# Optimization experiments

Measured on AMD Instinct MI355X. Metric: run time of the kernel, lower is better.

The kernel has to match this reference:

```python
import jax, jax.numpy as jnp
import numpy as np

NS, NM, NR, H = 5000, 100000, 2000, 128
E_SM, E_RM, E_SIM, L = 2_000_000, 1_000_000, 2_000_000, 500_000
NUM_LAYERS = 4  # flattened: layer-0 sage convs 0..3, layer-1 sage convs 0..3 -> stacked [2,4,...]


def _seg_sum(x, idx, n):
    return jax.ops.segment_sum(x, idx, num_segments=n)


def sage_conv(x_src, x_dst, Wl, bl, Wr, src, dst, n_dst):
    # PyG SAGEConv: mean-aggregate neighbor features, lin_l (with bias), + lin_r(root, no bias)
    agg = _seg_sum(x_src[src], dst, n_dst)                      # [n_dst, H]
    cnt = _seg_sum(jnp.ones_like(src, dtype=x_src.dtype), dst, n_dst)
    mean = agg / jnp.maximum(cnt, 1.0)[:, None]
    return mean @ Wl + bl + x_dst @ Wr


def gcn_conv(x, W, b, src, dst, n):
    # PyG GCNConv: add self loops, symmetric normalization deg^-1/2 (deg over dst incl. self loops)
    loop = jnp.arange(n, dtype=src.dtype)
    src2 = jnp.concatenate([src, loop])
    dst2 = jnp.concatenate([dst, loop])
    deg = _seg_sum(jnp.ones_like(dst2, dtype=x.dtype), dst2, n)
    dinv = jnp.where(deg > 0, jax.lax.rsqrt(deg), 0.0)
    norm = dinv[src2] * dinv[dst2]                               # [E+n]
    xw = x @ W                                                   # [n, H]
    out = _seg_sum(xw[src2] * norm[:, None], dst2, n)
    return out + b


def setup_inputs() -> dict:
    key = jax.random.key(0)
    ks = jax.random.split(key, 20)
    s = 0.05
    inp = {
        "emb_srna": jax.random.normal(ks[0], (NS, H), jnp.float32) * s,
        "emb_mrna": jax.random.normal(ks[1], (NM, H), jnp.float32) * s,
        "emb_rbp": jax.random.normal(ks[2], (NR, H), jnp.float32) * s,
        # stacked SAGE params: [layer=2, rel=4, ...]; rel order:
        # 0: srna->mrna, 1: mrna->srna (rev), 2: rbp->mrna, 3: mrna->rbp (rev)
        "sage_Wl": jax.random.normal(ks[3], (2, 4, H, H), jnp.float32) * s,
        "sage_bl": jnp.zeros((2, 4, H), jnp.float32),
        "sage_Wr": jax.random.normal(ks[4], (2, 4, H, H), jnp.float32) * s,
        # stacked GCN params: [layer=2, rel=2 (sim, rev_sim), ...]
        "gcn_W": jax.random.normal(ks[5], (2, 2, H, H), jnp.float32) * s,
        "gcn_b": jnp.zeros((2, 2, H), jnp.float32),
        "src_sm": jax.random.randint(ks[6], (E_SM,), 0, NS),
        "dst_sm": jax.random.randint(ks[7], (E_SM,), 0, NM),
        "src_rm": jax.random.randint(ks[8], (E_RM,), 0, NR),
        "dst_rm": jax.random.randint(ks[9], (E_RM,), 0, NM),
        "src_sim": jax.random.randint(ks[10], (E_SIM,), 0, NM),
        "dst_sim": jax.random.randint(ks[11], (E_SIM,), 0, NM),
        "lbl_srna": jax.random.randint(ks[12], (L,), 0, NS),
        "lbl_mrna": jax.random.randint(ks[13], (L,), 0, NM),
        "lbl_rbp": jax.random.randint(ks[14], (L,), 0, NR),
    }
    return inp


def reference(emb_srna, emb_mrna, emb_rbp, sage_Wl, sage_bl, sage_Wr, gcn_W, gcn_b,
              src_sm, dst_sm, src_rm, dst_rm, src_sim, dst_sim,
              lbl_srna, lbl_mrna, lbl_rbp):
    x_s, x_m, x_r = emb_srna, emb_mrna, emb_rbp
    for l in range(2):
        m_new = (
            sage_conv(x_s, x_m, sage_Wl[l, 0], sage_bl[l, 0], sage_Wr[l, 0], src_sm, dst_sm, NM)
            + sage_conv(x_r, x_m, sage_Wl[l, 2], sage_bl[l, 2], sage_Wr[l, 2], src_rm, dst_rm, NM)
            + gcn_conv(x_m, gcn_W[l, 0], gcn_b[l, 0], src_sim, dst_sim, NM)
            + gcn_conv(x_m, gcn_W[l, 1], gcn_b[l, 1], dst_sim, src_sim, NM)
        )
        s_new = sage_conv(x_m, x_s, sage_Wl[l, 1], sage_bl[l, 1], sage_Wr[l, 1], dst_sm, src_sm, NS)
        r_new = sage_conv(x_m, x_r, sage_Wl[l, 3], sage_bl[l, 3], sage_Wr[l, 3], dst_rm, src_rm, NR)
        x_s, x_m, x_r = jax.nn.relu(s_new), jax.nn.relu(m_new), jax.nn.relu(r_new)
    feat_m = x_m[lbl_mrna]
    pred_srna_mrna = jnp.sum(x_s[lbl_srna] * feat_m, axis=-1)
    pred_rbp_mrna = jnp.sum(x_r[lbl_rbp] * feat_m, axis=-1)
    return (pred_srna_mrna, pred_rbp_mrna)
```

## Files before the change

### kernel.cpp

```cpp
#include <hip/hip_runtime.h>
#include <hip/hip_bf16.h>

#define NSN 5000
#define NMN 100000
#define NRN 2000
#define HDIM 128
#define ESM 2000000
#define ERM 1000000
#define ESIM 2000000
#define LBL 500000

#define CNT_TOTAL (4 * NMN + NSN + NRN)
#define POOL_TOTAL (2 * ESM + 2 * ERM + 2 * ESIM)
#define NBTOT 1222
#define WCAP 14336
#define MAXNODES 512

typedef short bf16x8 __attribute__((ext_vector_type(8)));
typedef float f32x4 __attribute__((ext_vector_type(4)));

__device__ __forceinline__ unsigned short f2bf(float f) {
  unsigned u = __float_as_uint(f);
  unsigned r = (u + 0x7fffu + ((u >> 16) & 1u)) >> 16;
  return (unsigned short)r;
}
__device__ __forceinline__ float bf_lo(unsigned v) { return __uint_as_float(v << 16); }
__device__ __forceinline__ float bf_hi(unsigned v) { return __uint_as_float(v & 0xffff0000u); }
__device__ __forceinline__ unsigned pack2(float x, float y) {
  return (unsigned)f2bf(x) | ((unsigned)f2bf(y) << 16);
}
__device__ __forceinline__ void unpack8(uint4 v, float* f) {
  f[0] = bf_lo(v.x); f[1] = bf_hi(v.x);
  f[2] = bf_lo(v.y); f[3] = bf_hi(v.y);
  f[4] = bf_lo(v.z); f[5] = bf_hi(v.z);
  f[6] = bf_lo(v.w); f[7] = bf_hi(v.w);
}


__global__ void zero_int(int* __restrict__ p, int n) {
  int i = blockIdx.x * blockDim.x + threadIdx.x;
  if (i < n) p[i] = 0;
}

struct BInfo { int g; int ns; int ne; };
__device__ __forceinline__ BInfo binfo(int id) {
  BInfo bi;
  if (id < 196)       { int k = id;        bi.g = 0;                   bi.ns = k << 9; bi.ne = min(bi.ns + 512, NMN); }
  else if (id < 509)  { int k = id - 196;  bi.g = NMN;                 bi.ns = k << 4; bi.ne = min(bi.ns + 16,  NSN); }
  else if (id < 705)  { int k = id - 509;  bi.g = NMN + NSN;           bi.ns = k << 9; bi.ne = min(bi.ns + 512, NMN); }
  else if (id < 830)  { int k = id - 705;  bi.g = 2 * NMN + NSN;       bi.ns = k << 4; bi.ne = min(bi.ns + 16,  NRN); }
  else if (id < 1026) { int k = id - 830;  bi.g = 2 * NMN + NSN + NRN; bi.ns = k << 9; bi.ne = min(bi.ns + 512, NMN); }
  else                { int k = id - 1026; bi.g = 3 * NMN + NSN + NRN; bi.ns = k << 9; bi.ne = min(bi.ns + 512, NMN); }
  return bi;
}

template <int SHF, int NBF, int SHR, int NBR>
__global__ __launch_bounds__(256) void countbuckets(
    const int* __restrict__ a, const int* __restrict__ b, int n,
    int* __restrict__ bcnt, int bb) {
  __shared__ int hist[NBF + NBR];
  int tid = threadIdx.x;
  int base = blockIdx.x * 4096;
  for (int k = tid; k < NBF + NBR; k += 256) hist[k] = 0;
  __syncthreads();
  int end = min(base + 4096, n);
  for (int idx = base + tid; idx < end; idx += 256) {
    atomicAdd(&hist[b[idx] >> SHF], 1);
    atomicAdd(&hist[NBF + (a[idx] >> SHR)], 1);
  }
  __syncthreads();
  for (int k = tid; k < NBF + NBR; k += 256) {
    int c = hist[k];
    if (c) atomicAdd(&bcnt[bb + k], c);
  }
}

__global__ void scan_buckets(const int* __restrict__ bcnt, int* __restrict__ bstart,
                             int* __restrict__ bcur, int* __restrict__ off_sentinel) {
  __shared__ int buf[256];
  int t = threadIdx.x;
  int base = 0;
  for (int c0 = 0; c0 < NBTOT; c0 += 256) {
    int v = (c0 + t < NBTOT) ? bcnt[c0 + t] : 0;
    buf[t] = v; __syncthreads();
    for (int o = 1; o < 256; o <<= 1) {
      int a = (t >= o) ? buf[t - o] : 0;
      __syncthreads();
      buf[t] += a;
      __syncthreads();
    }
    if (c0 + t < NBTOT) {
      int excl = buf[t] - v + base;
      bstart[c0 + t] = excl;
      bcur[c0 + t] = excl;
    }
    base += buf[255];
    __syncthreads();
  }
  if (t == 0) { bstart[NBTOT] = base; *off_sentinel = base; }
}

template <int SHF, int NBF, int SHR, int NBR>
__global__ __launch_bounds__(256) void multisplit(
    const int* __restrict__ a, const int* __restrict__ b, int n,
    int* __restrict__ bcur, int bb, int* __restrict__ stage) {
  __shared__ int hist[NBF + NBR];
  __shared__ int gpos[NBF + NBR];
  int tid = threadIdx.x;
  int base = blockIdx.x * 4096;
  for (int k = tid; k < NBF + NBR; k += 256) hist[k] = 0;
  __syncthreads();
  int dv[16], sv[16];
#pragma unroll
  for (int j = 0; j < 16; j++) {
    int idx = base + j * 256 + tid;
    if (idx < n) {
      sv[j] = a[idx]; dv[j] = b[idx];
      atomicAdd(&hist[dv[j] >> SHF], 1);
      atomicAdd(&hist[NBF + (sv[j] >> SHR)], 1);
    } else {
      dv[j] = -1;
    }
  }
  __syncthreads();
  for (int k = tid; k < NBF + NBR; k += 256) {
    int c = hist[k];
    gpos[k] = c ? atomicAdd(&bcur[bb + k], c) : 0;
  }
  __syncthreads();
#pragma unroll
  for (int j = 0; j < 16; j++) {
    if (dv[j] >= 0) {
      int s1 = atomicAdd(&gpos[dv[j] >> SHF], 1);
      stage[2 * s1] = dv[j]; stage[2 * s1 + 1] = sv[j];
      int s2 = atomicAdd(&gpos[NBF + (sv[j] >> SHR)], 1);
      stage[2 * s2] = sv[j]; stage[2 * s2 + 1] = dv[j];
    }
  }
}

__global__ __launch_bounds__(256) void scatter_bucket(
    const int* __restrict__ stage, const int* __restrict__ bstart,
    int* __restrict__ cur, int* __restrict__ off, int* __restrict__ pool) {
  __shared__ int win[WCAP];
  __shared__ int hist[MAXNODES];
  __shared__ int part[256];
  int b = blockIdx.x;
  BInfo bi = binfo(b);
  int s0 = bstart[b], s1 = bstart[b + 1];
  int sz = s1 - s0, nn = bi.ne - bi.ns;
  int t = threadIdx.x;
  for (int k = t; k < nn; k += 256) hist[k] = 0;
  __syncthreads();
  for (int k = s0 + t; k < s1; k += 256)
    atomicAdd(&hist[stage[2 * k] - bi.ns], 1);
  __syncthreads();
  int a0 = (2 * t < nn) ? hist[2 * t] : 0;
  int a1 = (2 * t + 1 < nn) ? hist[2 * t + 1] : 0;
  part[t] = a0 + a1;
  __syncthreads();
  for (int o = 1; o < 256; o <<= 1) {
    int a = (t >= o) ? part[t - o] : 0;
    __syncthreads();
    part[t] += a;
    __syncthreads();
  }
  int e0 = part[t] - a0 - a1;
  int e1 = e0 + a0;
  if (2 * t < nn)     { off[bi.g + bi.ns + 2 * t] = s0 + e0; hist[2 * t] = e0; }
  if (2 * t + 1 < nn) { off[bi.g + bi.ns + 2 * t + 1] = s0 + e1; hist[2 * t + 1] = e1; }
  __syncthreads();
  if (sz <= WCAP) {
    for (int k = s0 + t; k < s1; k += 256) {
      int d = stage[2 * k], s_ = stage[2 * k + 1];
      int slot = atomicAdd(&hist[d - bi.ns], 1);
      win[slot] = s_;
    }
    __syncthreads();
    for (int k = t; k < sz; k += 256) pool[s0 + k] = win[k];
  } else {
    for (int k = s0 + t; k < s1; k += 256) {
      int d = stage[2 * k], s_ = stage[2 * k + 1];
      int slot = atomicAdd(&cur[bi.g + d], 1);
      pool[s0 + hist[d - bi.ns] + slot] = s_;
    }
  }
}

__global__ void compute_dinv(const int* __restrict__ off1, const int* __restrict__ off2,
                             float* __restrict__ dinv1, float* __restrict__ dinv2, int n) {
  int v = blockIdx.x * blockDim.x + threadIdx.x;
  if (v < n) {
    dinv1[v] = rsqrtf((float)(off1[v + 1] - off1[v] + 1));
    dinv2[v] = rsqrtf((float)(off2[v + 1] - off2[v] + 1));
  }
}

__global__ void trans_weights(const float* __restrict__ sWl, const float* __restrict__ sWr,
                              const float* __restrict__ gW, unsigned short* __restrict__ wt) {
  int i = blockIdx.x * blockDim.x + threadIdx.x;
  if (i >= 18 * 16384) return;
  int mat = i >> 14, l = mat / 9, slot = mat % 9;
  int idx = i & 16383, nn = idx >> 7, kk = idx & 127;
  int s_ = kk * 128 + nn;
  float v;
  if (slot < 4)      v = sWl[((l * 4 + slot) << 14) + s_];
  else if (slot < 6) v = gW[((l * 2 + (slot - 4)) << 14) + s_];
  else if (slot == 6) v = sWr[((l * 4 + 0) << 14) + s_] + sWr[((l * 4 + 2) << 14) + s_];
  else if (slot == 7) v = sWr[((l * 4 + 1) << 14) + s_];
  else                v = sWr[((l * 4 + 3) << 14) + s_];
  wt[i] = f2bf(v);
}

__global__ void prep_bias(const float* __restrict__ sbl, const float* __restrict__ gb,
                          float* __restrict__ biasM) {
  int i = threadIdx.x;
  int l = i >> 7, j = i & 127;
  biasM[i] = sbl[(l * 4 + 0) * 128 + j] + sbl[(l * 4 + 2) * 128 + j] +
             gb[(l * 2 + 0) * 128 + j] + gb[(l * 2 + 1) * 128 + j];
}

__global__ void cast_all(const float2* __restrict__ es, const float2* __restrict__ em,
                         const float2* __restrict__ er, unsigned* __restrict__ os,
                         unsigned* __restrict__ om, unsigned* __restrict__ orr) {
  int i = blockIdx.x * blockDim.x + threadIdx.x;
  if (i < NSN * 64) { float2 v = es[i]; os[i] = pack2(v.x, v.y); }
  if (i < NMN * 64) { float2 v = em[i]; om[i] = pack2(v.x, v.y); }
  if (i < NRN * 64) { float2 v = er[i]; orr[i] = pack2(v.x, v.y); }
}


__global__ void sage_agg(const unsigned* __restrict__ x, const int* __restrict__ pool,
                         const int* __restrict__ off, unsigned* __restrict__ outb, int n) {
  int w = (blockIdx.x * blockDim.x + threadIdx.x) >> 6;
  if (w >= n) return;
  int lane = threadIdx.x & 63;
  int q = lane >> 4, h = lane & 15;
  int s = off[w], e = off[w + 1];
  float acc[8];
#pragma unroll
  for (int j = 0; j < 8; j++) acc[j] = 0.f;
  for (int i0 = s; i0 < e; i0 += 8) {
    int iA = i0 + q, iB = i0 + 4 + q;
    int uA = pool[min(iA, e - 1)], uB = pool[min(iB, e - 1)];
    uint4 a = *(const uint4*)(x + (size_t)uA * 64 + h * 4);
    uint4 b = *(const uint4*)(x + (size_t)uB * 64 + h * 4);
    float sA = (iA < e) ? 1.f : 0.f, sB = (iB < e) ? 1.f : 0.f;
    float fa[8], fb[8];
    unpack8(a, fa); unpack8(b, fb);
#pragma unroll
    for (int j = 0; j < 8; j++) acc[j] = fmaf(fa[j], sA, fmaf(fb[j], sB, acc[j]));
  }
#pragma unroll
  for (int j = 0; j < 8; j++) {
    acc[j] += __shfl_xor(acc[j], 16, 64);
    acc[j] += __shfl_xor(acc[j], 32, 64);
  }
  if (q == 0) {
    float inv = (e > s) ? 1.0f / (float)(e - s) : 0.0f;
    uint4 o;
    o.x = pack2(acc[0] * inv, acc[1] * inv);
    o.y = pack2(acc[2] * inv, acc[3] * inv);
    o.z = pack2(acc[4] * inv, acc[5] * inv);
    o.w = pack2(acc[6] * inv, acc[7] * inv);
    *(uint4*)(outb + (size_t)w * 64 + h * 4) = o;
  }
}

__global__ void gcn_agg(const unsigned* __restrict__ x, const int* __restrict__ pool,
                        const int* __restrict__ off, const float* __restrict__ dinv,
                        unsigned* __restrict__ outb, int n) {
  int w = (blockIdx.x * blockDim.x + threadIdx.x) >> 6;
  if (w >= n) return;
  int lane = threadIdx.x & 63;
  int q = lane >> 4, h = lane & 15;
  int s = off[w], e = off[w + 1];
  float acc[8];
#pragma unroll
  for (int j = 0; j < 8; j++) acc[j] = 0.f;
  for (int i0 = s; i0 < e; i0 += 8) {
    int iA = i0 + q, iB = i0 + 4 + q;
    int uA = pool[min(iA, e - 1)], uB = pool[min(iB, e - 1)];
    uint4 a = *(const uint4*)(x + (size_t)uA * 64 + h * 4);
    uint4 b = *(const uint4*)(x + (size_t)uB * 64 + h * 4);
    float sA = (iA < e) ? dinv[uA] : 0.f, sB = (iB < e) ? dinv[uB] : 0.f;
    float fa[8], fb[8];
    unpack8(a, fa); unpack8(b, fb);
#pragma unroll
    for (int j = 0; j < 8; j++) acc[j] = fmaf(fa[j], sA, fmaf(fb[j], sB, acc[j]));
  }
#pragma unroll
  for (int j = 0; j < 8; j++) {
    acc[j] += __shfl_xor(acc[j], 16, 64);
    acc[j] += __shfl_xor(acc[j], 32, 64);
  }
  if (q == 0) {
    float dw = dinv[w];
    uint4 xv = *(const uint4*)(x + (size_t)w * 64 + h * 4);
    float fx[8];
    unpack8(xv, fx);
    uint4 o;
    float r0 = acc[0] * dw + fx[0] * dw * dw, r1 = acc[1] * dw + fx[1] * dw * dw;
    float r2 = acc[2] * dw + fx[2] * dw * dw, r3 = acc[3] * dw + fx[3] * dw * dw;
    float r4 = acc[4] * dw + fx[4] * dw * dw, r5 = acc[5] * dw + fx[5] * dw * dw;
    float r6 = acc[6] * dw + fx[6] * dw * dw, r7 = acc[7] * dw + fx[7] * dw * dw;
    o.x = pack2(r0, r1); o.y = pack2(r2, r3); o.z = pack2(r4, r5); o.w = pack2(r6, r7);
    *(uint4*)(outb + (size_t)w * 64 + h * 4) = o;
  }
}

__global__ __launch_bounds__(256) void sage_agg_mw(const unsigned* __restrict__ x,
                                                   const int* __restrict__ pool,
                                                   const int* __restrict__ off,
                                                   unsigned* __restrict__ outb, int n) {
  __shared__ float psum[3][128];
  int node = blockIdx.x;
  if (node >= n) return;
  int sub = threadIdx.x >> 6, lane = threadIdx.x & 63;
  int q = lane >> 4, h = lane & 15;
  int s = off[node], e = off[node + 1];
  float acc[8];
#pragma unroll
  for (int j = 0; j < 8; j++) acc[j] = 0.f;
  for (int i0 = s + sub * 4; i0 < e; i0 += 16) {
    int idx = i0 + q;
    int u = pool[min(idx, e - 1)];
    uint4 a = *(const uint4*)(x + (size_t)u * 64 + h * 4);
    float sc = (idx < e) ? 1.f : 0.f;
    float fa[8];
    unpack8(a, fa);
#pragma unroll
    for (int j = 0; j < 8; j++) acc[j] = fmaf(fa[j], sc, acc[j]);
  }
#pragma unroll
  for (int j = 0; j < 8; j++) {
    acc[j] += __shfl_xor(acc[j], 16, 64);
    acc[j] += __shfl_xor(acc[j], 32, 64);
  }
  if (sub && q == 0) {
#pragma unroll
    for (int j = 0; j < 8; j++) psum[sub - 1][h * 8 + j] = acc[j];
  }
  __syncthreads();
  if (sub == 0 && q == 0) {
#pragma unroll
    for (int j = 0; j < 8; j++)
      acc[j] += psum[0][h * 8 + j] + psum[1][h * 8 + j] + psum[2][h * 8 + j];
    float inv = (e > s) ? 1.0f / (float)(e - s) : 0.0f;
    uint4 o;
    o.x = pack2(acc[0] * inv, acc[1] * inv);
    o.y = pack2(acc[2] * inv, acc[3] * inv);
    o.z = pack2(acc[4] * inv, acc[5] * inv);
    o.w = pack2(acc[6] * inv, acc[7] * inv);
    *(uint4*)(outb + (size_t)node * 64 + h * 4) = o;
  }
}


#define LDA 136

__global__ __launch_bounds__(256) void gemm_mfma(
    const unsigned short* __restrict__ a0, const unsigned short* __restrict__ w0,
    const unsigned short* __restrict__ a1, const unsigned short* __restrict__ w1,
    const unsigned short* __restrict__ a2, const unsigned short* __restrict__ w2,
    const unsigned short* __restrict__ a3, const unsigned short* __restrict__ w3,
    const unsigned short* __restrict__ a4, const unsigned short* __restrict__ w4,
    const float* __restrict__ bias, unsigned short* __restrict__ out, int n) {
  __shared__ __align__(16) unsigned short As[64 * LDA];
  __shared__ __align__(16) unsigned short Ws[128 * LDA];

  int tid = threadIdx.x;
  int w = tid >> 6, lane = tid & 63;
  int q = lane >> 4, c = lane & 15;
  int r0 = blockIdx.x * 64;

  const unsigned short* Ap[5] = {a0, a1, a2, a3, a4};
  const unsigned short* Wp[5] = {w0, w1, w2, w3, w4};

  float bias_v[8];
#pragma unroll
  for (int n0 = 0; n0 < 8; n0++) bias_v[n0] = bias[n0 * 16 + c];

  f32x4 acc[8];
#pragma unroll
  for (int n0 = 0; n0 < 8; n0++) acc[n0] = (f32x4){0.f, 0.f, 0.f, 0.f};

  for (int p = 0; p < 5; p++) {
    if (!Ap[p]) continue;
    __syncthreads();
    for (int j = tid; j < 2048; j += 256) {
      int row = j >> 4, colc = (j & 15) * 8;
      *(uint4*)&Ws[row * LDA + colc] = *(const uint4*)(Wp[p] + row * 128 + colc);
    }
    for (int j = tid; j < 1024; j += 256) {
      int row = j >> 4, colc = (j & 15) * 8;
      uint4 v = make_uint4(0u, 0u, 0u, 0u);
      if (r0 + row < n) v = *(const uint4*)(Ap[p] + (size_t)(r0 + row) * 128 + colc);
      *(uint4*)&As[row * LDA + colc] = v;
    }
    __syncthreads();

    int arow = (w * 16 + c) * LDA;
#pragma unroll
    for (int k0 = 0; k0 < 128; k0 += 32) {
      bf16x8 af = *(const bf16x8*)&As[arow + k0 + q * 8];
#pragma unroll
      for (int n0 = 0; n0 < 8; n0++) {
        bf16x8 bfv = *(const bf16x8*)&Ws[(n0 * 16 + c) * LDA + k0 + q * 8];
        acc[n0] = __builtin_amdgcn_mfma_f32_16x16x32_bf16(af, bfv, acc[n0], 0, 0, 0);
      }
    }
  }

  __syncthreads();
#pragma unroll
  for (int n0 = 0; n0 < 8; n0++) {
#pragma unroll
    for (int reg = 0; reg < 4; reg++) {
      float v = acc[n0][reg] + bias_v[n0];
      v = fmaxf(v, 0.f);
      As[(w * 16 + q * 4 + reg) * LDA + n0 * 16 + c] = f2bf(v);
    }
  }
  __syncthreads();
  for (int j = tid; j < 1024; j += 256) {
    int row = j >> 4, colc = (j & 15) * 8;
    if (r0 + row < n)
      *(uint4*)(out + (size_t)(r0 + row) * 128 + colc) = *(const uint4*)&As[row * LDA + colc];
  }
}


__global__ void dots_kernel(const unsigned* __restrict__ xs, const unsigned* __restrict__ xm,
                            const unsigned* __restrict__ xr, const int* __restrict__ ls,
                            const int* __restrict__ lm, const int* __restrict__ lr,
                            float* __restrict__ out) {
  int wv = (blockIdx.x * blockDim.x + threadIdx.x) >> 6;
  int lane = threadIdx.x & 63;
  int q = lane >> 4, h = lane & 15;
  int i = wv * 4 + q;
  if (i >= LBL) return;
  int im = lm[i], is = ls[i], ir = lr[i];
  uint4 mv = *(const uint4*)(xm + (size_t)im * 64 + h * 4);
  uint4 sv = *(const uint4*)(xs + (size_t)is * 64 + h * 4);
  uint4 rv = *(const uint4*)(xr + (size_t)ir * 64 + h * 4);
  float fm[8], fs[8], fr[8];
  unpack8(mv, fm); unpack8(sv, fs); unpack8(rv, fr);
  float p1 = 0.f, p2 = 0.f;
#pragma unroll
  for (int j = 0; j < 8; j++) { p1 = fmaf(fs[j], fm[j], p1); p2 = fmaf(fr[j], fm[j], p2); }
#pragma unroll
  for (int m = 1; m < 16; m <<= 1) {
    p1 += __shfl_xor(p1, m, 64);
    p2 += __shfl_xor(p2, m, 64);
  }
  if (h == 0) { out[i] = p1; out[LBL + i] = p2; }
}


extern "C" void kernel_launch(void* const* d_in, const int* in_sizes, int n_in,
                              void* d_out, int out_size, void* d_ws, size_t ws_size,
                              hipStream_t stream) {
  const float* emb_s = (const float*)d_in[0];
  const float* emb_m = (const float*)d_in[1];
  const float* emb_r = (const float*)d_in[2];
  const float* sWl = (const float*)d_in[3];
  const float* sbl = (const float*)d_in[4];
  const float* sWr = (const float*)d_in[5];
  const float* gW  = (const float*)d_in[6];
  const float* gb  = (const float*)d_in[7];
  const int* src_sm  = (const int*)d_in[8];
  const int* dst_sm  = (const int*)d_in[9];
  const int* src_rm  = (const int*)d_in[10];
  const int* dst_rm  = (const int*)d_in[11];
  const int* src_sim = (const int*)d_in[12];
  const int* dst_sim = (const int*)d_in[13];
  const int* lbl_s = (const int*)d_in[14];
  const int* lbl_m = (const int*)d_in[15];
  const int* lbl_r = (const int*)d_in[16];
  float* out = (float*)d_out;

  char* p = (char*)d_ws;
  auto alloc = [&](size_t bytes) -> char* {
    char* r = p;
    p += (bytes + 255) & ~(size_t)255;
    return r;
  };

  int* cnt_base = (int*)alloc(sizeof(int) * CNT_TOTAL);

  int* off_base = (int*)alloc(sizeof(int) * (CNT_TOTAL + 1));
  int* off_sm  = off_base;
  int* off_ms  = off_sm + NMN;
  int* off_rm  = off_ms + NSN;
  int* off_mr  = off_rm + NMN;
  int* off_si  = off_mr + NRN;
  int* off_si2 = off_si + NMN;

  int* bcnt   = (int*)alloc(sizeof(int) * 1280);
  int* bstart = (int*)alloc(sizeof(int) * 1280);
  int* bcur   = (int*)alloc(sizeof(int) * 1280);
  int* pool = (int*)alloc(sizeof(int) * POOL_TOTAL);

  float* dinv1 = (float*)alloc(sizeof(float) * NMN);
  float* dinv2 = (float*)alloc(sizeof(float) * NMN);

  unsigned* xsb = (unsigned*)alloc(sizeof(unsigned) * (size_t)NSN * 64);
  unsigned* xmb = (unsigned*)alloc(sizeof(unsigned) * (size_t)NMN * 64);
  unsigned* xrb = (unsigned*)alloc(sizeof(unsigned) * (size_t)NRN * 64);
  unsigned* xs0 = (unsigned*)alloc(sizeof(unsigned) * (size_t)NSN * 64);
  unsigned* xs1 = (unsigned*)alloc(sizeof(unsigned) * (size_t)NSN * 64);
  unsigned* xm0 = (unsigned*)alloc(sizeof(unsigned) * (size_t)NMN * 64);
  unsigned* xm1 = (unsigned*)alloc(sizeof(unsigned) * (size_t)NMN * 64);
  unsigned* xr0 = (unsigned*)alloc(sizeof(unsigned) * (size_t)NRN * 64);
  unsigned* xr1 = (unsigned*)alloc(sizeof(unsigned) * (size_t)NRN * 64);
  unsigned* aggA = (unsigned*)alloc(sizeof(unsigned) * (size_t)NMN * 64);
  unsigned* aggB = (unsigned*)alloc(sizeof(unsigned) * (size_t)NMN * 64);
  unsigned* aggC = (unsigned*)alloc(sizeof(unsigned) * (size_t)NMN * 64);
  unsigned* aggD = (unsigned*)alloc(sizeof(unsigned) * (size_t)NMN * 64);

  unsigned short* wt = (unsigned short*)alloc(sizeof(unsigned short) * 18 * 16384);
  float* biasM = (float*)alloc(sizeof(float) * 2 * 128);

  int* stage = (int*)aggA;

  auto WT = [&](int l, int slot) -> const unsigned short* {
    return wt + (((size_t)l * 9 + slot) << 14);
  };

  zero_int<<<5, 256, 0, stream>>>(bcnt, 1280);
  countbuckets<9, 196, 4, 313><<<(ESM + 4095) / 4096, 256, 0, stream>>>(
      src_sm, dst_sm, ESM, bcnt, 0);
  countbuckets<9, 196, 4, 125><<<(ERM + 4095) / 4096, 256, 0, stream>>>(
      src_rm, dst_rm, ERM, bcnt, 509);
  countbuckets<9, 196, 9, 196><<<(ESIM + 4095) / 4096, 256, 0, stream>>>(
      src_sim, dst_sim, ESIM, bcnt, 830);
  scan_buckets<<<1, 256, 0, stream>>>(bcnt, bstart, bcur, off_base + CNT_TOTAL);

  multisplit<9, 196, 4, 313><<<(ESM + 4095) / 4096, 256, 0, stream>>>(
      src_sm, dst_sm, ESM, bcur, 0, stage);
  multisplit<9, 196, 4, 125><<<(ERM + 4095) / 4096, 256, 0, stream>>>(
      src_rm, dst_rm, ERM, bcur, 509, stage);
  multisplit<9, 196, 9, 196><<<(ESIM + 4095) / 4096, 256, 0, stream>>>(
      src_sim, dst_sim, ESIM, bcur, 830, stage);
  zero_int<<<(CNT_TOTAL + 255) / 256, 256, 0, stream>>>(cnt_base, CNT_TOTAL);
  scatter_bucket<<<NBTOT, 256, 0, stream>>>(stage, bstart, cnt_base, off_base, pool);

  compute_dinv<<<(NMN + 255) / 256, 256, 0, stream>>>(off_si, off_si2, dinv1, dinv2, NMN);
  trans_weights<<<(18 * 16384 + 255) / 256, 256, 0, stream>>>(sWl, sWr, gW, wt);
  prep_bias<<<1, 256, 0, stream>>>(sbl, gb, biasM);
  cast_all<<<(NMN * 64 + 255) / 256, 256, 0, stream>>>((const float2*)emb_s, (const float2*)emb_m,
                                                       (const float2*)emb_r, xsb, xmb, xrb);

  for (int l = 0; l < 2; ++l) {
    const unsigned* xs_c = l ? xs0 : xsb;
    const unsigned* xm_c = l ? xm0 : xmb;
    const unsigned* xr_c = l ? xr0 : xrb;
    unsigned* xs_n = l ? xs1 : xs0;
    unsigned* xm_n = l ? xm1 : xm0;
    unsigned* xr_n = l ? xr1 : xr0;

    sage_agg<<<(NMN + 3) / 4, 256, 0, stream>>>(xs_c, pool, off_sm, aggA, NMN);
    sage_agg<<<(NMN + 3) / 4, 256, 0, stream>>>(xr_c, pool, off_rm, aggB, NMN);
    gcn_agg<<<(NMN + 3) / 4, 256, 0, stream>>>(xm_c, pool, off_si, dinv1, aggC, NMN);
    gcn_agg<<<(NMN + 3) / 4, 256, 0, stream>>>(xm_c, pool, off_si2, dinv2, aggD, NMN);
    gemm_mfma<<<(NMN + 63) / 64, 256, 0, stream>>>(
        (const unsigned short*)aggA, WT(l, 0), (const unsigned short*)aggB, WT(l, 2),
        (const unsigned short*)aggC, WT(l, 4), (const unsigned short*)aggD, WT(l, 5),
        (const unsigned short*)xm_c, WT(l, 6), biasM + l * 128,
        (unsigned short*)xm_n, NMN);

    sage_agg_mw<<<NSN, 256, 0, stream>>>(xm_c, pool, off_ms, aggA, NSN);
    gemm_mfma<<<(NSN + 63) / 64, 256, 0, stream>>>(
        (const unsigned short*)aggA, WT(l, 1), (const unsigned short*)xs_c, WT(l, 7),
        nullptr, nullptr, nullptr, nullptr, nullptr, nullptr,
        sbl + (l * 4 + 1) * 128, (unsigned short*)xs_n, NSN);

    sage_agg_mw<<<NRN, 256, 0, stream>>>(xm_c, pool, off_mr, aggB, NRN);
    gemm_mfma<<<(NRN + 63) / 64, 256, 0, stream>>>(
        (const unsigned short*)aggB, WT(l, 3), (const unsigned short*)xr_c, WT(l, 8),
        nullptr, nullptr, nullptr, nullptr, nullptr, nullptr,
        sbl + (l * 4 + 3) * 128, (unsigned short*)xr_n, NRN);
  }

  dots_kernel<<<(LBL * 16 + 255) / 256, 256, 0, stream>>>(xs1, xm1, xr1, lbl_s, lbl_m, lbl_r, out);
}
```

Baseline: 1.242 ms.

## Fuse all per-layer aggregation kernels into one launch and vectorize stage pairs

Merges the four mRNA-destination aggregations (two SAGE, two GCN) and the sRNA/RBP multi-wave aggregations into a single agg_all kernel per layer. Each mRNA wave now handles all four relations for its node, and extra blocks handle the sRNA and RBP nodes. This cuts launches and lets the small-node aggregations run concurrently with the large ones, but it adds per-wave serial work and separate aggS/aggR buffers. The multisplit stage buffer is also changed to int2 so each staged pair is written and read as one 8-byte access.

Measured after the change: 1.185 ms. 1.05x faster.

```diff
diff --git a/kernel.cpp b/kernel.cpp
--- a/kernel.cpp
+++ b/kernel.cpp
@@ -15,6 +15,7 @@
 #define NBTOT 1222
 #define WCAP 14336
 #define MAXNODES 512
+#define MBLK 25000
 
 typedef short bf16x8 __attribute__((ext_vector_type(8)));
 typedef float f32x4 __attribute__((ext_vector_type(4)));
@@ -103,7 +104,7 @@
 template <int SHF, int NBF, int SHR, int NBR>
 __global__ __launch_bounds__(256) void multisplit(
     const int* __restrict__ a, const int* __restrict__ b, int n,
-    int* __restrict__ bcur, int bb, int* __restrict__ stage) {
+    int* __restrict__ bcur, int bb, int2* __restrict__ stage) {
   __shared__ int hist[NBF + NBR];
   __shared__ int gpos[NBF + NBR];
   int tid = threadIdx.x;
@@ -132,15 +133,15 @@
   for (int j = 0; j < 16; j++) {
     if (dv[j] >= 0) {
       int s1 = atomicAdd(&gpos[dv[j] >> SHF], 1);
-      stage[2 * s1] = dv[j]; stage[2 * s1 + 1] = sv[j];
+      stage[s1] = make_int2(dv[j], sv[j]);
       int s2 = atomicAdd(&gpos[NBF + (sv[j] >> SHR)], 1);
-      stage[2 * s2] = sv[j]; stage[2 * s2 + 1] = dv[j];
+      stage[s2] = make_int2(sv[j], dv[j]);
     }
   }
 }
 
 __global__ __launch_bounds__(256) void scatter_bucket(
-    const int* __restrict__ stage, const int* __restrict__ bstart,
+    const int2* __restrict__ stage, const int* __restrict__ bstart,
     int* __restrict__ cur, int* __restrict__ off, int* __restrict__ pool) {
   __shared__ int win[WCAP];
   __shared__ int hist[MAXNODES];
@@ -153,7 +154,7 @@
   for (int k = t; k < nn; k += 256) hist[k] = 0;
   __syncthreads();
   for (int k = s0 + t; k < s1; k += 256)
-    atomicAdd(&hist[stage[2 * k] - bi.ns], 1);
+    atomicAdd(&hist[stage[k].x - bi.ns], 1);
   __syncthreads();
   int a0 = (2 * t < nn) ? hist[2 * t] : 0;
   int a1 = (2 * t + 1 < nn) ? hist[2 * t + 1] : 0;
@@ -172,17 +173,17 @@
   __syncthreads();
   if (sz <= WCAP) {
     for (int k = s0 + t; k < s1; k += 256) {
-      int d = stage[2 * k], s_ = stage[2 * k + 1];
-      int slot = atomicAdd(&hist[d - bi.ns], 1);
-      win[slot] = s_;
+      int2 pr = stage[k];
+      int slot = atomicAdd(&hist[pr.x - bi.ns], 1);
+      win[slot] = pr.y;
     }
     __syncthreads();
     for (int k = t; k < sz; k += 256) pool[s0 + k] = win[k];
   } else {
     for (int k = s0 + t; k < s1; k += 256) {
-      int d = stage[2 * k], s_ = stage[2 * k + 1];
-      int slot = atomicAdd(&cur[bi.g + d], 1);
-      pool[s0 + hist[d - bi.ns] + slot] = s_;
+      int2 pr = stage[k];
+      int slot = atomicAdd(&cur[bi.g + pr.x], 1);
+      pool[s0 + hist[pr.x - bi.ns] + slot] = pr.y;
     }
   }
 }
@@ -230,16 +231,9 @@
 }
 
 
-__global__ void sage_agg(const unsigned* __restrict__ x, const int* __restrict__ pool,
-                         const int* __restrict__ off, unsigned* __restrict__ outb, int n) {
-  int w = (blockIdx.x * blockDim.x + threadIdx.x) >> 6;
-  if (w >= n) return;
-  int lane = threadIdx.x & 63;
-  int q = lane >> 4, h = lane & 15;
-  int s = off[w], e = off[w + 1];
-  float acc[8];
-#pragma unroll
-  for (int j = 0; j < 8; j++) acc[j] = 0.f;
+__device__ __forceinline__ void gsum_plain(const unsigned* __restrict__ x,
+                                           const int* __restrict__ pool, int s, int e,
+                                           int q, int h, float* acc) {
   for (int i0 = s; i0 < e; i0 += 8) {
     int iA = i0 + q, iB = i0 + 4 + q;
     int uA = pool[min(iA, e - 1)], uB = pool[min(iB, e - 1)];
@@ -251,33 +245,12 @@
 #pragma unroll
     for (int j = 0; j < 8; j++) acc[j] = fmaf(fa[j], sA, fmaf(fb[j], sB, acc[j]));
   }
-#pragma unroll
-  for (int j = 0; j < 8; j++) {
-    acc[j] += __shfl_xor(acc[j], 16, 64);
-    acc[j] += __shfl_xor(acc[j], 32, 64);
-  }
-  if (q == 0) {
-    float inv = (e > s) ? 1.0f / (float)(e - s) : 0.0f;
-    uint4 o;
-    o.x = pack2(acc[0] * inv, acc[1] * inv);
-    o.y = pack2(acc[2] * inv, acc[3] * inv);
-    o.z = pack2(acc[4] * inv, acc[5] * inv);
-    o.w = pack2(acc[6] * inv, acc[7] * inv);
-    *(uint4*)(outb + (size_t)w * 64 + h * 4) = o;
-  }
-}
-
-__global__ void gcn_agg(const unsigned* __restrict__ x, const int* __restrict__ pool,
-                        const int* __restrict__ off, const float* __restrict__ dinv,
-                        unsigned* __restrict__ outb, int n) {
-  int w = (blockIdx.x * blockDim.x + threadIdx.x) >> 6;
-  if (w >= n) return;
-  int lane = threadIdx.x & 63;
-  int q = lane >> 4, h = lane & 15;
-  int s = off[w], e = off[w + 1];
-  float acc[8];
-#pragma unroll
-  for (int j = 0; j < 8; j++) acc[j] = 0.f;
+}
+
+__device__ __forceinline__ void gsum_gcn(const unsigned* __restrict__ x,
+                                         const int* __restrict__ pool,
+                                         const float* __restrict__ dinv, int s, int e,
+                                         int q, int h, float* acc) {
   for (int i0 = s; i0 < e; i0 += 8) {
     int iA = i0 + q, iB = i0 + 4 + q;
     int uA = pool[min(iA, e - 1)], uB = pool[min(iB, e - 1)];
@@ -289,70 +262,144 @@
 #pragma unroll
     for (int j = 0; j < 8; j++) acc[j] = fmaf(fa[j], sA, fmaf(fb[j], sB, acc[j]));
   }
+}
+
+__device__ __forceinline__ void wave_reduce(float* acc) {
 #pragma unroll
   for (int j = 0; j < 8; j++) {
     acc[j] += __shfl_xor(acc[j], 16, 64);
     acc[j] += __shfl_xor(acc[j], 32, 64);
   }
-  if (q == 0) {
-    float dw = dinv[w];
-    uint4 xv = *(const uint4*)(x + (size_t)w * 64 + h * 4);
-    float fx[8];
-    unpack8(xv, fx);
-    uint4 o;
-    float r0 = acc[0] * dw + fx[0] * dw * dw, r1 = acc[1] * dw + fx[1] * dw * dw;
-    float r2 = acc[2] * dw + fx[2] * dw * dw, r3 = acc[3] * dw + fx[3] * dw * dw;
-    float r4 = acc[4] * dw + fx[4] * dw * dw, r5 = acc[5] * dw + fx[5] * dw * dw;
-    float r6 = acc[6] * dw + fx[6] * dw * dw, r7 = acc[7] * dw + fx[7] * dw * dw;
-    o.x = pack2(r0, r1); o.y = pack2(r2, r3); o.z = pack2(r4, r5); o.w = pack2(r6, r7);
-    *(uint4*)(outb + (size_t)w * 64 + h * 4) = o;
-  }
-}
-
-__global__ __launch_bounds__(256) void sage_agg_mw(const unsigned* __restrict__ x,
-                                                   const int* __restrict__ pool,
-                                                   const int* __restrict__ off,
-                                                   unsigned* __restrict__ outb, int n) {
+}
+
+__global__ __launch_bounds__(256) void agg_all(
+    const unsigned* __restrict__ xs, const unsigned* __restrict__ xm,
+    const unsigned* __restrict__ xr, const int* __restrict__ pool,
+    const int* __restrict__ off_sm, const int* __restrict__ off_rm,
+    const int* __restrict__ off_si, const int* __restrict__ off_si2,
+    const int* __restrict__ off_ms, const int* __restrict__ off_mr,
+    const float* __restrict__ dinv1, const float* __restrict__ dinv2,
+    unsigned* __restrict__ aggA, unsigned* __restrict__ aggB,
+    unsigned* __restrict__ aggC, unsigned* __restrict__ aggD,
+    unsigned* __restrict__ aggS, unsigned* __restrict__ aggR) {
   __shared__ float psum[3][128];
-  int node = blockIdx.x;
-  if (node >= n) return;
-  int sub = threadIdx.x >> 6, lane = threadIdx.x & 63;
+  int b = blockIdx.x;
+  int lane = threadIdx.x & 63;
   int q = lane >> 4, h = lane & 15;
-  int s = off[node], e = off[node + 1];
-  float acc[8];
-#pragma unroll
-  for (int j = 0; j < 8; j++) acc[j] = 0.f;
-  for (int i0 = s + sub * 4; i0 < e; i0 += 16) {
-    int idx = i0 + q;
-    int u = pool[min(idx, e - 1)];
-    uint4 a = *(const uint4*)(x + (size_t)u * 64 + h * 4);
-    float sc = (idx < e) ? 1.f : 0.f;
-    float fa[8];
-    unpack8(a, fa);
-#pragma unroll
-    for (int j = 0; j < 8; j++) acc[j] = fmaf(fa[j], sc, acc[j]);
-  }
-#pragma unroll
-  for (int j = 0; j < 8; j++) {
-    acc[j] += __shfl_xor(acc[j], 16, 64);
-    acc[j] += __shfl_xor(acc[j], 32, 64);
-  }
-  if (sub && q == 0) {
-#pragma unroll
-    for (int j = 0; j < 8; j++) psum[sub - 1][h * 8 + j] = acc[j];
-  }
-  __syncthreads();
-  if (sub == 0 && q == 0) {
-#pragma unroll
-    for (int j = 0; j < 8; j++)
-      acc[j] += psum[0][h * 8 + j] + psum[1][h * 8 + j] + psum[2][h * 8 + j];
-    float inv = (e > s) ? 1.0f / (float)(e - s) : 0.0f;
-    uint4 o;
-    o.x = pack2(acc[0] * inv, acc[1] * inv);
-    o.y = pack2(acc[2] * inv, acc[3] * inv);
-    o.z = pack2(acc[4] * inv, acc[5] * inv);
-    o.w = pack2(acc[6] * inv, acc[7] * inv);
-    *(uint4*)(outb + (size_t)node * 64 + h * 4) = o;
+
+  if (b < MBLK) {
+    int w = b * 4 + (threadIdx.x >> 6);
+    if (w >= NMN) return;
+    float acc[8];
+    {
+      int s = off_sm[w], e = off_sm[w + 1];
+#pragma unroll
+      for (int j = 0; j < 8; j++) acc[j] = 0.f;
+      gsum_plain(xs, pool, s, e, q, h, acc);
+      wave_reduce(acc);
+      if (q == 0) {
+        float inv = (e > s) ? 1.0f / (float)(e - s) : 0.0f;
+        uint4 o;
+        o.x = pack2(acc[0] * inv, acc[1] * inv);
+        o.y = pack2(acc[2] * inv, acc[3] * inv);
+        o.z = pack2(acc[4] * inv, acc[5] * inv);
+        o.w = pack2(acc[6] * inv, acc[7] * inv);
+        *(uint4*)(aggA + (size_t)w * 64 + h * 4) = o;
+      }
+    }
+    {
+      int s = off_rm[w], e = off_rm[w + 1];
+#pragma unroll
+      for (int j = 0; j < 8; j++) acc[j] = 0.f;
+      gsum_plain(xr, pool, s, e, q, h, acc);
+      wave_reduce(acc);
+      if (q == 0) {
+        float inv = (e > s) ? 1.0f / (float)(e - s) : 0.0f;
+        uint4 o;
+        o.x = pack2(acc[0] * inv, acc[1] * inv);
+        o.y = pack2(acc[2] * inv, acc[3] * inv);
+        o.z = pack2(acc[4] * inv, acc[5] * inv);
+        o.w = pack2(acc[6] * inv, acc[7] * inv);
+        *(uint4*)(aggB + (size_t)w * 64 + h * 4) = o;
+      }
+    }
+    {
+      int s = off_si[w], e = off_si[w + 1];
+#pragma unroll
+      for (int j = 0; j < 8; j++) acc[j] = 0.f;
+      gsum_gcn(xm, pool, dinv1, s, e, q, h, acc);
+      wave_reduce(acc);
+      if (q == 0) {
+        float dw = dinv1[w];
+        uint4 xv = *(const uint4*)(xm + (size_t)w * 64 + h * 4);
+        float fx[8];
+        unpack8(xv, fx);
+        uint4 o;
+        o.x = pack2(acc[0] * dw + fx[0] * dw * dw, acc[1] * dw + fx[1] * dw * dw);
+        o.y = pack2(acc[2] * dw + fx[2] * dw * dw, acc[3] * dw + fx[3] * dw * dw);
+        o.z = pack2(acc[4] * dw + fx[4] * dw * dw, acc[5] * dw + fx[5] * dw * dw);
+        o.w = pack2(acc[6] * dw + fx[6] * dw * dw, acc[7] * dw + fx[7] * dw * dw);
+        *(uint4*)(aggC + (size_t)w * 64 + h * 4) = o;
+      }
+    }
+    {
+      int s = off_si2[w], e = off_si2[w + 1];
+#pragma unroll
+      for (int j = 0; j < 8; j++) acc[j] = 0.f;
+      gsum_gcn(xm, pool, dinv2, s, e, q, h, acc);
+      wave_reduce(acc);
+      if (q == 0) {
+        float dw = dinv2[w];
+        uint4 xv = *(const uint4*)(xm + (size_t)w * 64 + h * 4);
+        float fx[8];
+        unpack8(xv, fx);
+        uint4 o;
+        o.x = pack2(acc[0] * dw + fx[0] * dw * dw, acc[1] * dw + fx[1] * dw * dw);
+        o.y = pack2(acc[2] * dw + fx[2] * dw * dw, acc[3] * dw + fx[3] * dw * dw);
+        o.z = pack2(acc[4] * dw + fx[4] * dw * dw, acc[5] * dw + fx[5] * dw * dw);
+        o.w = pack2(acc[6] * dw + fx[6] * dw * dw, acc[7] * dw + fx[7] * dw * dw);
+        *(uint4*)(aggD + (size_t)w * 64 + h * 4) = o;
+      }
+    }
+  } else {
+    int node;
+    const int* offp;
+    unsigned* outb;
+    if (b < MBLK + NSN) { node = b - MBLK; offp = off_ms; outb = aggS; }
+    else                { node = b - MBLK - NSN; offp = off_mr; outb = aggR; }
+    int sub = threadIdx.x >> 6;
+    int s = offp[node], e = offp[node + 1];
+    float acc[8];
+#pragma unroll
+    for (int j = 0; j < 8; j++) acc[j] = 0.f;
+    for (int i0 = s + sub * 4; i0 < e; i0 += 16) {
+      int idx = i0 + q;
+      int u = pool[min(idx, e - 1)];
+      uint4 a = *(const uint4*)(xm + (size_t)u * 64 + h * 4);
+      float sc = (idx < e) ? 1.f : 0.f;
+      float fa[8];
+      unpack8(a, fa);
+#pragma unroll
+      for (int j = 0; j < 8; j++) acc[j] = fmaf(fa[j], sc, acc[j]);
+    }
+    wave_reduce(acc);
+    if (sub && q == 0) {
+#pragma unroll
+      for (int j = 0; j < 8; j++) psum[sub - 1][h * 8 + j] = acc[j];
+    }
+    __syncthreads();
+    if (sub == 0 && q == 0) {
+#pragma unroll
+      for (int j = 0; j < 8; j++)
+        acc[j] += psum[0][h * 8 + j] + psum[1][h * 8 + j] + psum[2][h * 8 + j];
+      float inv = (e > s) ? 1.0f / (float)(e - s) : 0.0f;
+      uint4 o;
+      o.x = pack2(acc[0] * inv, acc[1] * inv);
+      o.y = pack2(acc[2] * inv, acc[3] * inv);
+      o.z = pack2(acc[4] * inv, acc[5] * inv);
+      o.w = pack2(acc[6] * inv, acc[7] * inv);
+      *(uint4*)(outb + (size_t)node * 64 + h * 4) = o;
+    }
   }
 }
 
@@ -518,11 +565,13 @@
   unsigned* aggB = (unsigned*)alloc(sizeof(unsigned) * (size_t)NMN * 64);
   unsigned* aggC = (unsigned*)alloc(sizeof(unsigned) * (size_t)NMN * 64);
   unsigned* aggD = (unsigned*)alloc(sizeof(unsigned) * (size_t)NMN * 64);
+  unsigned* aggS = (unsigned*)alloc(sizeof(unsigned) * (size_t)NSN * 64);
+  unsigned* aggR = (unsigned*)alloc(sizeof(unsigned) * (size_t)NRN * 64);
 
   unsigned short* wt = (unsigned short*)alloc(sizeof(unsigned short) * 18 * 16384);
   float* biasM = (float*)alloc(sizeof(float) * 2 * 128);
 
-  int* stage = (int*)aggA;
+  int2* stage = (int2*)aggA;
 
   auto WT = [&](int l, int slot) -> const unsigned short* {
     return wt + (((size_t)l * 9 + slot) << 14);
@@ -552,6 +601,7 @@
   cast_all<<<(NMN * 64 + 255) / 256, 256, 0, stream>>>((const float2*)emb_s, (const float2*)emb_m,
                                                        (const float2*)emb_r, xsb, xmb, xrb);
 
+  const int AGG_GRID = MBLK + NSN + NRN;
   for (int l = 0; l < 2; ++l) {
     const unsigned* xs_c = l ? xs0 : xsb;
     const unsigned* xm_c = l ? xm0 : xmb;
@@ -560,25 +610,21 @@
     unsigned* xm_n = l ? xm1 : xm0;
     unsigned* xr_n = l ? xr1 : xr0;
 
-    sage_agg<<<(NMN + 3) / 4, 256, 0, stream>>>(xs_c, pool, off_sm, aggA, NMN);
-    sage_agg<<<(NMN + 3) / 4, 256, 0, stream>>>(xr_c, pool, off_rm, aggB, NMN);
-    gcn_agg<<<(NMN + 3) / 4, 256, 0, stream>>>(xm_c, pool, off_si, dinv1, aggC, NMN);
-    gcn_agg<<<(NMN + 3) / 4, 256, 0, stream>>>(xm_c, pool, off_si2, dinv2, aggD, NMN);
+    agg_all<<<AGG_GRID, 256, 0, stream>>>(
+        xs_c, xm_c, xr_c, pool, off_sm, off_rm, off_si, off_si2, off_ms, off_mr,
+        dinv1, dinv2, aggA, aggB, aggC, aggD, aggS, aggR);
+
     gemm_mfma<<<(NMN + 63) / 64, 256, 0, stream>>>(
         (const unsigned short*)aggA, WT(l, 0), (const unsigned short*)aggB, WT(l, 2),
         (const unsigned short*)aggC, WT(l, 4), (const unsigned short*)aggD, WT(l, 5),
         (const unsigned short*)xm_c, WT(l, 6), biasM + l * 128,
         (unsigned short*)xm_n, NMN);
-
-    sage_agg_mw<<<NSN, 256, 0, stream>>>(xm_c, pool, off_ms, aggA, NSN);
     gemm_mfma<<<(NSN + 63) / 64, 256, 0, stream>>>(
-        (const unsigned short*)aggA, WT(l, 1), (const unsigned short*)xs_c, WT(l, 7),
+        (const unsigned short*)aggS, WT(l, 1), (const unsigned short*)xs_c, WT(l, 7),
         nullptr, nullptr, nullptr, nullptr, nullptr, nullptr,
         sbl + (l * 4 + 1) * 128, (unsigned short*)xs_n, NSN);
-
-    sage_agg_mw<<<NRN, 256, 0, stream>>>(xm_c, pool, off_mr, aggB, NRN);
     gemm_mfma<<<(NRN + 63) / 64, 256, 0, stream>>>(
-        (const unsigned short*)aggB, WT(l, 3), (const unsigned short*)xr_c, WT(l, 8),
+        (const unsigned short*)aggR, WT(l, 3), (const unsigned short*)xr_c, WT(l, 8),
         nullptr, nullptr, nullptr, nullptr, nullptr, nullptr,
         sbl + (l * 4 + 3) * 128, (unsigned short*)xr_n, NRN);
   }
```
